# Kernel tuning notes

Hardware: AMD Instinct MI355X
Metric: run time of the kernel (lower is better)

Reference implementation:

```python
import jax, jax.numpy as jnp
import numpy as np

N_USERS = 100000
N_ENT = 100000
DIM = 64
HID = 128
E = 1600000
B = 8192


def _renorm(emb, max_norm=1.0):
    # torch nn.Embedding(max_norm=1): rows are rescaled to norm <= max_norm on lookup
    n = jnp.linalg.norm(emb, axis=-1, keepdims=True)
    return emb * jnp.minimum(1.0, max_norm / jnp.maximum(n, 1e-12))


def _gcn_conv(x, W, b, src, dst, n):
    # PyG GCNConv: h = x W; add self-loops; sym-normalized scatter-add; + bias
    h = x @ W  # [n, out]
    deg = jax.ops.segment_sum(jnp.ones(src.shape, jnp.float32), dst, num_segments=n) + 1.0  # self-loop
    dinv = jax.lax.rsqrt(deg)
    norm = (dinv[src] * dinv[dst])[:, None]  # [E,1]
    out = jax.ops.segment_sum(h[src] * norm, dst, num_segments=n)
    out = out + h * (1.0 / deg)[:, None]  # self-loop term: deg^-1/2 * deg^-1/2 = 1/deg
    return out + b


def setup_inputs() -> dict:
    key = jax.random.key(0)
    ks = jax.random.split(key, 8)
    return {
        "u": jax.random.randint(ks[0], (B,), 0, N_USERS),
        "i": jax.random.randint(ks[1], (B,), 0, N_ENT),
        "edges": jax.random.randint(ks[2], (2, E), 0, N_ENT),
        "user_emb": jax.random.normal(ks[3], (N_USERS, DIM), jnp.float32) * 0.1,
        "entity_emb": jax.random.normal(ks[4], (N_ENT, DIM), jnp.float32) * 0.1,
        "W1": jax.random.normal(ks[5], (DIM, HID), jnp.float32) * (1.0 / np.sqrt(DIM)),
        "b1": jnp.zeros((HID,), jnp.float32),
        "W2": jax.random.normal(ks[6], (HID, DIM), jnp.float32) * (1.0 / np.sqrt(HID)),
        "b2": jnp.zeros((DIM,), jnp.float32),
    }


def reference(u, i, edges, user_emb, entity_emb, W1, b1, W2, b2):
    src, dst = edges[0], edges[1]
    n = entity_emb.shape[0]
    x = _renorm(entity_emb)  # entitys(all_entitys_indexes) with max_norm=1
    x = jax.nn.relu(_gcn_conv(x, W1, b1, src, dst, n))  # dropout = identity (eval)
    x = _gcn_conv(x, W2, b2, src, dst, n)
    items = x[i]  # [B, DIM]
    users = _renorm(user_emb)[u]  # [B, DIM]
    uv = jnp.sum(users * items, axis=1)
    return jax.nn.sigmoid(uv)
```

## Files before the change

kernel.cpp:

```cpp
#include <hip/hip_runtime.h>
#include <hip/hip_bf16.h>
#include <math.h>

constexpr int N_ENT = 100000;
constexpr int NEDGE = 1600000;
constexpr int BATCH = 8192;

constexpr int NBUCK   = 256;
constexpr int KNODE   = 391;
constexpr int TILE    = 4096;
constexpr int NTILE   = (NEDGE + TILE - 1) / TILE;
constexpr int BUCKCAP = 8192;

constexpr int NBLK_G = (N_ENT + 63) / 64;
constexpr int ZROWS  = NBLK_G * 64;


typedef __attribute__((ext_vector_type(8))) short bf16x8;
typedef __attribute__((ext_vector_type(4))) float f32x4;

__device__ inline unsigned short f2b(float x) {
    unsigned int u = __float_as_uint(x);
    unsigned int r = (u + 0x7fffu + ((u >> 16) & 1u)) >> 16;
    return (unsigned short)r;
}
__device__ inline float blo(unsigned int p) { return __uint_as_float(p << 16); }
__device__ inline float bhi(unsigned int p) { return __uint_as_float(p & 0xffff0000u); }


__global__ __launch_bounds__(256) void prep_k(const float* __restrict__ emb,
                                              const int* __restrict__ degi,
                                              float* __restrict__ dinv,
                                              unsigned short* __restrict__ emb_b) {
    int gt   = blockIdx.x * 256 + threadIdx.x;
    int n    = gt >> 6;
    int lane = threadIdx.x & 63;
    if (n > N_ENT) return;
    if (n == N_ENT) { emb_b[(size_t)n * 64 + lane] = 0; return; }
    float v = emb[(size_t)n * 64 + lane];
    float s = v * v;
#pragma unroll
    for (int o = 32; o > 0; o >>= 1) s += __shfl_xor(s, o, 64);
    float nrm = sqrtf(s);
    float sc  = nrm > 1.0f ? 1.0f / nrm : 1.0f;
    float dv  = 1.0f / sqrtf((float)(degi[n] + 1));
    if (lane == 0) dinv[n] = dv;
    emb_b[(size_t)n * 64 + lane] = f2b(sc * dv * v);
}

__global__ __launch_bounds__(256) void init_k(const float* __restrict__ W1g,
                                              const float* __restrict__ W2g,
                                              uint4* __restrict__ w1p,
                                              uint4* __restrict__ w2p,
                                              int* __restrict__ gcursor) {
    if (blockIdx.x == 8) { gcursor[threadIdx.x] = threadIdx.x * BUCKCAP; return; }
    int t = blockIdx.x * 256 + threadIdx.x;
    int e    = t & 1023;
    int lane = e & 63, cs = e >> 6;
    int li   = lane & 15, quad = lane >> 4;
    unsigned short v[8];
    if (t < 1024) {
        int ct = cs >> 1, s = cs & 1;
        int kb = s * 32 + quad * 8;
        int n  = ct * 16 + li;
#pragma unroll
        for (int j = 0; j < 8; ++j) v[j] = f2b(W1g[(kb + j) * 128 + n]);
        uint4 p;
        p.x = (unsigned)v[0] | ((unsigned)v[1] << 16);
        p.y = (unsigned)v[2] | ((unsigned)v[3] << 16);
        p.z = (unsigned)v[4] | ((unsigned)v[5] << 16);
        p.w = (unsigned)v[6] | ((unsigned)v[7] << 16);
        w1p[e] = p;
    } else {
        int ct = cs >> 2, s = cs & 3;
        int kb = s * 32 + quad * 8;
        int n  = ct * 16 + li;
#pragma unroll
        for (int j = 0; j < 8; ++j) v[j] = f2b(W2g[(kb + j) * 64 + n]);
        uint4 p;
        p.x = (unsigned)v[0] | ((unsigned)v[1] << 16);
        p.y = (unsigned)v[2] | ((unsigned)v[3] << 16);
        p.z = (unsigned)v[4] | ((unsigned)v[5] << 16);
        p.w = (unsigned)v[6] | ((unsigned)v[7] << 16);
        w2p[e] = p;
    }
}

__global__ __launch_bounds__(256) void bin_k(const int* __restrict__ edges,
                                             int* __restrict__ gcursor,
                                             unsigned int* __restrict__ temp) {
    __shared__ int cnt[NBUCK];
    __shared__ int gb[NBUCK];
    __shared__ int off[NBUCK];
    int tid  = threadIdx.x;
    int base = blockIdx.x * TILE;
    unsigned int val[16];
    unsigned int bpk[4] = {0u, 0u, 0u, 0u};
    cnt[tid] = 0;
    __syncthreads();
#pragma unroll
    for (int i = 0; i < 16; ++i) {
        int e = base + i * 256 + tid;
        unsigned int b = 0u;
        if (e < NEDGE) {
            int s  = edges[e];
            int d  = edges[NEDGE + e];
            int bb = d / KNODE;
            int dl = d - bb * KNODE;
            val[i] = ((unsigned int)s << 9) | (unsigned int)dl;
            b = (unsigned int)bb;
            atomicAdd(&cnt[bb], 1);
        } else {
            val[i] = 0xffffffffu;
        }
        bpk[i >> 2] |= b << ((i & 3) * 8);
    }
    __syncthreads();
    if (cnt[tid] > 0) gb[tid] = atomicAdd(&gcursor[tid], cnt[tid]);
    off[tid] = 0;
    __syncthreads();
#pragma unroll
    for (int i = 0; i < 16; ++i) {
        if (val[i] != 0xffffffffu) {
            int b = (int)((bpk[i >> 2] >> ((i & 3) * 8)) & 255u);
            int p = atomicAdd(&off[b], 1);
            temp[gb[b] + p] = val[i];
        }
    }
}

__global__ __launch_bounds__(256) void count_k(const unsigned int* __restrict__ temp,
                                               const int* __restrict__ gcursor,
                                               int* __restrict__ degi) {
    __shared__ int cnt[KNODE];
    int b     = blockIdx.x;
    int node0 = b * KNODE;
    int nn    = N_ENT - node0; if (nn > KNODE) nn = KNODE;
    for (int i = threadIdx.x; i < KNODE; i += 256) cnt[i] = 0;
    __syncthreads();
    int tbeg = b * BUCKCAP;
    int tend = gcursor[b];
    for (int idx = tbeg + threadIdx.x; idx < tend; idx += 256)
        atomicAdd(&cnt[temp[idx] & 511u], 1);
    __syncthreads();
    for (int i = threadIdx.x; i < nn; i += 256) degi[node0 + i] = cnt[i];
}

__global__ __launch_bounds__(256) void scan_offsets(const int* __restrict__ gcursor,
                                                    int* __restrict__ bucket_base,
                                                    int* __restrict__ row_start) {
    __shared__ int ts[NBUCK];
    int t = threadIdx.x;
    int v = gcursor[t] - t * BUCKCAP;
    ts[t] = v;
    __syncthreads();
    for (int off = 1; off < NBUCK; off <<= 1) {
        int x = (t >= off) ? ts[t - off] : 0;
        __syncthreads();
        ts[t] += x;
        __syncthreads();
    }
    bucket_base[t] = ts[t] - v;
    if (t == 0) row_start[N_ENT] = NEDGE;
}

__global__ __launch_bounds__(256) void unbin_k(const unsigned int* __restrict__ temp,
                                               const int* __restrict__ gcursor,
                                               const int* __restrict__ bucket_base,
                                               const int* __restrict__ degi,
                                               int* __restrict__ row_start,
                                               int* __restrict__ srcs) {
    __shared__ int cur[KNODE];
    int b     = blockIdx.x;
    int node0 = b * KNODE;
    int nn    = N_ENT - node0; if (nn > KNODE) nn = KNODE;
    int tid   = threadIdx.x;
    if (tid < 64) {
        int lane = tid;
        int loc[7];
        int s = 0;
#pragma unroll
        for (int j = 0; j < 7; ++j) {
            int idx = lane * 7 + j;
            int d = (idx < nn) ? degi[node0 + idx] : 0;
            loc[j] = s;
            s += d;
        }
        int v = s;
#pragma unroll
        for (int o = 1; o < 64; o <<= 1) {
            int x = __shfl_up(v, o, 64);
            if (lane >= o) v += x;
        }
        int pfx  = v - s;
        int base = bucket_base[b];
#pragma unroll
        for (int j = 0; j < 7; ++j) {
            int idx = lane * 7 + j;
            if (idx < nn) {
                int rs = base + pfx + loc[j];
                cur[idx] = rs;
                row_start[node0 + idx] = rs;
            }
        }
    }
    __syncthreads();
    int tbeg = b * BUCKCAP;
    int tend = gcursor[b];
    for (int idx = tbeg + tid; idx < tend; idx += 256) {
        unsigned int v = temp[idx];
        int dl = (int)(v & 511u);
        int s  = (int)(v >> 9);
        int pos = atomicAdd(&cur[dl], 1);
        srcs[pos] = s;
    }
}

__global__ __launch_bounds__(256) void reduce1_k(const int* __restrict__ row_start,
                                                 const int* __restrict__ srcs,
                                                 const unsigned short* __restrict__ emb_b,
                                                 const float* __restrict__ dinv,
                                                 unsigned short* __restrict__ zb) {
    int gt   = blockIdx.x * 256 + threadIdx.x;
    int dst  = gt >> 6;
    int lane = threadIdx.x & 63;
    int sub  = lane >> 4;
    int li   = lane & 15;
    int beg = row_start[dst];
    int end = row_start[dst + 1];
    float4 acc = make_float4(0.f, 0.f, 0.f, 0.f);
    for (int base = beg; base < end; base += 64) {
        int cnt = end - base; if (cnt > 64) cnt = 64;
        int s_v = (base + lane < end) ? srcs[base + lane] : N_ENT;
        for (int jj = 0; jj < cnt; jj += 16) {
            int s0 = __shfl(s_v, jj + sub,      64);
            int s1 = __shfl(s_v, jj + 4 + sub,  64);
            int s2 = __shfl(s_v, jj + 8 + sub,  64);
            int s3 = __shfl(s_v, jj + 12 + sub, 64);
            uint2 p0 = *(const uint2*)(emb_b + (size_t)s0 * 64 + li * 4);
            uint2 p1 = *(const uint2*)(emb_b + (size_t)s1 * 64 + li * 4);
            uint2 p2 = *(const uint2*)(emb_b + (size_t)s2 * 64 + li * 4);
            uint2 p3 = *(const uint2*)(emb_b + (size_t)s3 * 64 + li * 4);
            acc.x += blo(p0.x) + blo(p1.x) + blo(p2.x) + blo(p3.x);
            acc.y += bhi(p0.x) + bhi(p1.x) + bhi(p2.x) + bhi(p3.x);
            acc.z += blo(p0.y) + blo(p1.y) + blo(p2.y) + blo(p3.y);
            acc.w += bhi(p0.y) + bhi(p1.y) + bhi(p2.y) + bhi(p3.y);
        }
    }
    acc.x += __shfl_xor(acc.x, 16, 64); acc.y += __shfl_xor(acc.y, 16, 64);
    acc.z += __shfl_xor(acc.z, 16, 64); acc.w += __shfl_xor(acc.w, 16, 64);
    acc.x += __shfl_xor(acc.x, 32, 64); acc.y += __shfl_xor(acc.y, 32, 64);
    acc.z += __shfl_xor(acc.z, 32, 64); acc.w += __shfl_xor(acc.w, 32, 64);
    if (lane < 16) {
        uint2 po = *(const uint2*)(emb_b + (size_t)dst * 64 + li * 4);
        float dv = dinv[dst];
        unsigned int h0 = f2b(dv * (acc.x + blo(po.x)));
        unsigned int h1 = f2b(dv * (acc.y + bhi(po.x)));
        unsigned int h2 = f2b(dv * (acc.z + blo(po.y)));
        unsigned int h3 = f2b(dv * (acc.w + bhi(po.y)));
        uint2 p;
        p.x = h0 | (h1 << 16);
        p.y = h2 | (h3 << 16);
        *(uint2*)(zb + (size_t)dst * 64 + li * 4) = p;
    }
}

__global__ __launch_bounds__(256) void mlp_k(const unsigned short* __restrict__ zb,
                                             const uint4* __restrict__ w1p,
                                             const float* __restrict__ b1,
                                             const uint4* __restrict__ w2p,
                                             const float* __restrict__ dinv,
                                             unsigned short* __restrict__ h2b) {
    __shared__ unsigned short y1s[4][16 * 136];
    __shared__ unsigned short h2s[4][16 * 64];
    int tid  = threadIdx.x;
    int w    = tid >> 6, lane = tid & 63;
    int li   = lane & 15, quad = lane >> 4;
    int r0   = blockIdx.x * 64 + w * 16;
    uint4 a0u = *(const uint4*)(zb + (size_t)(r0 + li) * 64 + quad * 8);
    uint4 a1u = *(const uint4*)(zb + (size_t)(r0 + li) * 64 + 32 + quad * 8);
    bf16x8 a0 = *(bf16x8*)&a0u;
    bf16x8 a1 = *(bf16x8*)&a1u;
    unsigned short* ys = y1s[w];
#pragma unroll
    for (int ct = 0; ct < 8; ++ct) {
        uint4 b0u = w1p[(ct * 2 + 0) * 64 + lane];
        uint4 b1u = w1p[(ct * 2 + 1) * 64 + lane];
        f32x4 acc = {0.f, 0.f, 0.f, 0.f};
        acc = __builtin_amdgcn_mfma_f32_16x16x32_bf16(a0, *(bf16x8*)&b0u, acc, 0, 0, 0);
        acc = __builtin_amdgcn_mfma_f32_16x16x32_bf16(a1, *(bf16x8*)&b1u, acc, 0, 0, 0);
        float bias = b1[ct * 16 + li];
#pragma unroll
        for (int r = 0; r < 4; ++r)
            ys[(quad * 4 + r) * 136 + ct * 16 + li] = f2b(fmaxf(acc[r] + bias, 0.f));
    }
    __syncthreads();
    bf16x8 a2[4];
#pragma unroll
    for (int s = 0; s < 4; ++s) {
        uint4 au = *(const uint4*)(ys + li * 136 + s * 32 + quad * 8);
        a2[s] = *(bf16x8*)&au;
    }
    float dvr[4];
#pragma unroll
    for (int r = 0; r < 4; ++r) {
        int grow = r0 + quad * 4 + r;
        dvr[r] = (grow < N_ENT) ? dinv[grow] : 0.f;
    }
    unsigned short* hs = h2s[w];
#pragma unroll
    for (int ct = 0; ct < 4; ++ct) {
        f32x4 acc = {0.f, 0.f, 0.f, 0.f};
#pragma unroll
        for (int s = 0; s < 4; ++s) {
            uint4 bu = w2p[(ct * 4 + s) * 64 + lane];
            acc = __builtin_amdgcn_mfma_f32_16x16x32_bf16(a2[s], *(bf16x8*)&bu, acc, 0, 0, 0);
        }
#pragma unroll
        for (int r = 0; r < 4; ++r)
            hs[(quad * 4 + r) * 64 + ct * 16 + li] = f2b(acc[r] * dvr[r]);
    }
    __syncthreads();
#pragma unroll
    for (int q = 0; q < 2; ++q) {
        int t4   = lane * 2 + q;
        int rl   = t4 >> 3;
        int c0   = (t4 & 7) * 8;
        int grow = r0 + rl;
        if (grow < N_ENT) {
            *(uint4*)(h2b + (size_t)grow * 64 + c0) = *(const uint4*)(hs + rl * 64 + c0);
        } else if (grow == N_ENT) {
            uint4 zz; zz.x = 0u; zz.y = 0u; zz.z = 0u; zz.w = 0u;
            *(uint4*)(h2b + (size_t)grow * 64 + c0) = zz;
        }
    }
}

__global__ __launch_bounds__(256) void reduce2f_k(const int* __restrict__ u,
                                                  const int* __restrict__ iidx,
                                                  const float* __restrict__ uemb,
                                                  const int* __restrict__ row_start,
                                                  const int* __restrict__ srcs,
                                                  const unsigned short* __restrict__ h2b,
                                                  const float* __restrict__ dinv,
                                                  const float* __restrict__ b2,
                                                  float* __restrict__ out) {
    int gt   = blockIdx.x * 256 + threadIdx.x;
    int b    = gt >> 6;
    int lane = threadIdx.x & 63;
    int sub  = lane >> 4;
    int li   = lane & 15;
    int dst = iidx[b];
    int beg = row_start[dst];
    int end = row_start[dst + 1];
    float4 acc = make_float4(0.f, 0.f, 0.f, 0.f);
    for (int base = beg; base < end; base += 64) {
        int cnt = end - base; if (cnt > 64) cnt = 64;
        int s_v = (base + lane < end) ? srcs[base + lane] : N_ENT;
        for (int jj = 0; jj < cnt; jj += 16) {
            int s0 = __shfl(s_v, jj + sub,      64);
            int s1 = __shfl(s_v, jj + 4 + sub,  64);
            int s2 = __shfl(s_v, jj + 8 + sub,  64);
            int s3 = __shfl(s_v, jj + 12 + sub, 64);
            uint2 p0 = *(const uint2*)(h2b + (size_t)s0 * 64 + li * 4);
            uint2 p1 = *(const uint2*)(h2b + (size_t)s1 * 64 + li * 4);
            uint2 p2 = *(const uint2*)(h2b + (size_t)s2 * 64 + li * 4);
            uint2 p3 = *(const uint2*)(h2b + (size_t)s3 * 64 + li * 4);
            acc.x += blo(p0.x) + blo(p1.x) + blo(p2.x) + blo(p3.x);
            acc.y += bhi(p0.x) + bhi(p1.x) + bhi(p2.x) + bhi(p3.x);
            acc.z += blo(p0.y) + blo(p1.y) + blo(p2.y) + blo(p3.y);
            acc.w += bhi(p0.y) + bhi(p1.y) + bhi(p2.y) + bhi(p3.y);
        }
    }
    acc.x += __shfl_xor(acc.x, 16, 64); acc.y += __shfl_xor(acc.y, 16, 64);
    acc.z += __shfl_xor(acc.z, 16, 64); acc.w += __shfl_xor(acc.w, 16, 64);
    acc.x += __shfl_xor(acc.x, 32, 64); acc.y += __shfl_xor(acc.y, 32, 64);
    acc.z += __shfl_xor(acc.z, 32, 64); acc.w += __shfl_xor(acc.w, 32, 64);
    float s1 = 0.f, s2 = 0.f;
    if (lane < 16) {
        uint2 po = *(const uint2*)(h2b + (size_t)dst * 64 + li * 4);
        float dv = dinv[dst];
        float4 bb = *(const float4*)(b2 + li * 4);
        float4 z2v;
        z2v.x = dv * (acc.x + blo(po.x)) + bb.x;
        z2v.y = dv * (acc.y + bhi(po.x)) + bb.y;
        z2v.z = dv * (acc.z + blo(po.y)) + bb.z;
        z2v.w = dv * (acc.w + bhi(po.y)) + bb.w;
        float4 ue = *(const float4*)(uemb + (size_t)u[b] * 64 + li * 4);
        s1 = ue.x * ue.x + ue.y * ue.y + ue.z * ue.z + ue.w * ue.w;
        s2 = ue.x * z2v.x + ue.y * z2v.y + ue.z * z2v.z + ue.w * z2v.w;
    }
#pragma unroll
    for (int o = 8; o > 0; o >>= 1) {
        s1 += __shfl_xor(s1, o, 64);
        s2 += __shfl_xor(s2, o, 64);
    }
    if (lane == 0) {
        float nrm = sqrtf(s1);
        float sc  = nrm > 1.0f ? 1.0f / nrm : 1.0f;
        float uv  = s2 * sc;
        out[b] = 1.0f / (1.0f + expf(-uv));
    }
}

extern "C" void kernel_launch(void* const* d_in, const int* in_sizes, int n_in,
                              void* d_out, int out_size, void* d_ws, size_t ws_size,
                              hipStream_t stream) {
    const int*   u          = (const int*)d_in[0];
    const int*   iidx       = (const int*)d_in[1];
    const int*   edges      = (const int*)d_in[2];
    const float* user_emb   = (const float*)d_in[3];
    const float* entity_emb = (const float*)d_in[4];
    const float* W1         = (const float*)d_in[5];
    const float* b1         = (const float*)d_in[6];
    const float* W2         = (const float*)d_in[7];
    const float* b2         = (const float*)d_in[8];
    float*       out        = (float*)d_out;

    char* ws = (char*)d_ws;
    int*            degi        = (int*)           (ws);
    float*          dinv        = (float*)         (ws + 100000u * 4);
    int*            row_start   = (int*)           (ws + 200000u * 4);
    int*            gcursor     = (int*)           (ws + 300004u * 4);
    int*            bucket_base = (int*)           (ws + 300264u * 4);
    uint4*          w1p         = (uint4*)         (ws + 300656u * 4);
    uint4*          w2p         = (uint4*)         (ws + 304752u * 4);
    int*            srcs        = (int*)           (ws + 308848u * 4);
    unsigned short* emb_b       = (unsigned short*)(ws + 1908848u * 4);
    unsigned short* zb          = (unsigned short*)(ws + 3508864u * 4);
    unsigned short* h2b         = (unsigned short*)(ws + 6711936u * 4);
    unsigned int*   temp        = (unsigned int*)  (ws + 8311968u * 4);

    init_k<<<9, 256, 0, stream>>>(W1, W2, w1p, w2p, gcursor);
    bin_k<<<NTILE, 256, 0, stream>>>(edges, gcursor, temp);
    count_k<<<NBUCK, 256, 0, stream>>>(temp, gcursor, degi);
    scan_offsets<<<1, 256, 0, stream>>>(gcursor, bucket_base, row_start);

    prep_k<<<N_ENT * 64 / 256 + 1, 256, 0, stream>>>(entity_emb, degi, dinv, emb_b);

    unbin_k<<<NBUCK, 256, 0, stream>>>(temp, gcursor, bucket_base, degi,
                                       row_start, srcs);

    reduce1_k<<<N_ENT * 64 / 256, 256, 0, stream>>>(row_start, srcs, emb_b, dinv, zb);
    mlp_k<<<NBLK_G, 256, 0, stream>>>(zb, w1p, b1, w2p, dinv, h2b);

    reduce2f_k<<<BATCH * 64 / 256, 256, 0, stream>>>(u, iidx, user_emb, row_start,
                                                     srcs, h2b, dinv, b2, out);
}
```

Before: 238.2 us.

## Fuse count, scan and unbin into one LDS-staged kernel; derive degree from row_start

Merges the per-bucket degree count, global bucket scan and unbin scatter into a single kernel. Each block recomputes the 256-entry prefix scan redundantly and stages its bucket in LDS, so temp is read once instead of twice. Weight packing moves into extra blocks of the same launch, and degrees are taken from row_start differences, which drops the degi array. This removes several launches and a global round trip, at the cost of 32KB LDS per block, which may lower occupancy. reduce1 is also split into two launches over halves of the nodes.

```diff
diff --git a/kernel.cpp b/kernel.cpp
--- a/kernel.cpp
+++ b/kernel.cpp
@@ -28,62 +28,8 @@
 __device__ inline float bhi(unsigned int p) { return __uint_as_float(p & 0xffff0000u); }
 
 
-__global__ __launch_bounds__(256) void prep_k(const float* __restrict__ emb,
-                                              const int* __restrict__ degi,
-                                              float* __restrict__ dinv,
-                                              unsigned short* __restrict__ emb_b) {
-    int gt   = blockIdx.x * 256 + threadIdx.x;
-    int n    = gt >> 6;
-    int lane = threadIdx.x & 63;
-    if (n > N_ENT) return;
-    if (n == N_ENT) { emb_b[(size_t)n * 64 + lane] = 0; return; }
-    float v = emb[(size_t)n * 64 + lane];
-    float s = v * v;
-#pragma unroll
-    for (int o = 32; o > 0; o >>= 1) s += __shfl_xor(s, o, 64);
-    float nrm = sqrtf(s);
-    float sc  = nrm > 1.0f ? 1.0f / nrm : 1.0f;
-    float dv  = 1.0f / sqrtf((float)(degi[n] + 1));
-    if (lane == 0) dinv[n] = dv;
-    emb_b[(size_t)n * 64 + lane] = f2b(sc * dv * v);
-}
-
-__global__ __launch_bounds__(256) void init_k(const float* __restrict__ W1g,
-                                              const float* __restrict__ W2g,
-                                              uint4* __restrict__ w1p,
-                                              uint4* __restrict__ w2p,
-                                              int* __restrict__ gcursor) {
-    if (blockIdx.x == 8) { gcursor[threadIdx.x] = threadIdx.x * BUCKCAP; return; }
-    int t = blockIdx.x * 256 + threadIdx.x;
-    int e    = t & 1023;
-    int lane = e & 63, cs = e >> 6;
-    int li   = lane & 15, quad = lane >> 4;
-    unsigned short v[8];
-    if (t < 1024) {
-        int ct = cs >> 1, s = cs & 1;
-        int kb = s * 32 + quad * 8;
-        int n  = ct * 16 + li;
-#pragma unroll
-        for (int j = 0; j < 8; ++j) v[j] = f2b(W1g[(kb + j) * 128 + n]);
-        uint4 p;
-        p.x = (unsigned)v[0] | ((unsigned)v[1] << 16);
-        p.y = (unsigned)v[2] | ((unsigned)v[3] << 16);
-        p.z = (unsigned)v[4] | ((unsigned)v[5] << 16);
-        p.w = (unsigned)v[6] | ((unsigned)v[7] << 16);
-        w1p[e] = p;
-    } else {
-        int ct = cs >> 2, s = cs & 3;
-        int kb = s * 32 + quad * 8;
-        int n  = ct * 16 + li;
-#pragma unroll
-        for (int j = 0; j < 8; ++j) v[j] = f2b(W2g[(kb + j) * 64 + n]);
-        uint4 p;
-        p.x = (unsigned)v[0] | ((unsigned)v[1] << 16);
-        p.y = (unsigned)v[2] | ((unsigned)v[3] << 16);
-        p.z = (unsigned)v[4] | ((unsigned)v[5] << 16);
-        p.w = (unsigned)v[6] | ((unsigned)v[7] << 16);
-        w2p[e] = p;
-    }
+__global__ __launch_bounds__(256) void ginit_k(int* __restrict__ gcursor) {
+    gcursor[threadIdx.x] = threadIdx.x * BUCKCAP;
 }
 
 __global__ __launch_bounds__(256) void bin_k(const int* __restrict__ edges,
@@ -129,52 +75,76 @@
     }
 }
 
-__global__ __launch_bounds__(256) void count_k(const unsigned int* __restrict__ temp,
-                                               const int* __restrict__ gcursor,
-                                               int* __restrict__ degi) {
+__global__ __launch_bounds__(256) void unbinC_k(const unsigned int* __restrict__ temp,
+                                                const int* __restrict__ gcursor,
+                                                const float* __restrict__ W1g,
+                                                const float* __restrict__ W2g,
+                                                uint4* __restrict__ w1p,
+                                                uint4* __restrict__ w2p,
+                                                int* __restrict__ row_start,
+                                                int* __restrict__ srcs) {
+    __shared__ unsigned int st[BUCKCAP];
+    __shared__ int bs[NBUCK];
     __shared__ int cnt[KNODE];
-    int b     = blockIdx.x;
+    __shared__ int cur[KNODE];
+    int b   = blockIdx.x;
+    int tid = threadIdx.x;
+    if (b >= NBUCK) {
+        int t    = (b - NBUCK) * 256 + tid;
+        int e    = t & 1023;
+        int lane = e & 63, cs = e >> 6;
+        int li   = lane & 15, quad = lane >> 4;
+        unsigned short v[8];
+        if (t < 1024) {
+            int ct = cs >> 1, s = cs & 1;
+            int kb = s * 32 + quad * 8;
+            int n  = ct * 16 + li;
+#pragma unroll
+            for (int j = 0; j < 8; ++j) v[j] = f2b(W1g[(kb + j) * 128 + n]);
+            uint4 p;
+            p.x = (unsigned)v[0] | ((unsigned)v[1] << 16);
+            p.y = (unsigned)v[2] | ((unsigned)v[3] << 16);
+            p.z = (unsigned)v[4] | ((unsigned)v[5] << 16);
+            p.w = (unsigned)v[6] | ((unsigned)v[7] << 16);
+            w1p[e] = p;
+        } else {
+            int ct = cs >> 2, s = cs & 3;
+            int kb = s * 32 + quad * 8;
+            int n  = ct * 16 + li;
+#pragma unroll
+            for (int j = 0; j < 8; ++j) v[j] = f2b(W2g[(kb + j) * 64 + n]);
+            uint4 p;
+            p.x = (unsigned)v[0] | ((unsigned)v[1] << 16);
+            p.y = (unsigned)v[2] | ((unsigned)v[3] << 16);
+            p.z = (unsigned)v[4] | ((unsigned)v[5] << 16);
+            p.w = (unsigned)v[6] | ((unsigned)v[7] << 16);
+            w2p[e] = p;
+        }
+        return;
+    }
+    int myc = gcursor[tid] - tid * BUCKCAP;
+    bs[tid] = myc;
+    __syncthreads();
+    for (int off = 1; off < NBUCK; off <<= 1) {
+        int x = (tid >= off) ? bs[tid - off] : 0;
+        __syncthreads();
+        bs[tid] += x;
+        __syncthreads();
+    }
     int node0 = b * KNODE;
     int nn    = N_ENT - node0; if (nn > KNODE) nn = KNODE;
-    for (int i = threadIdx.x; i < KNODE; i += 256) cnt[i] = 0;
-    __syncthreads();
-    int tbeg = b * BUCKCAP;
-    int tend = gcursor[b];
-    for (int idx = tbeg + threadIdx.x; idx < tend; idx += 256)
-        atomicAdd(&cnt[temp[idx] & 511u], 1);
-    __syncthreads();
-    for (int i = threadIdx.x; i < nn; i += 256) degi[node0 + i] = cnt[i];
-}
-
-__global__ __launch_bounds__(256) void scan_offsets(const int* __restrict__ gcursor,
-                                                    int* __restrict__ bucket_base,
-                                                    int* __restrict__ row_start) {
-    __shared__ int ts[NBUCK];
-    int t = threadIdx.x;
-    int v = gcursor[t] - t * BUCKCAP;
-    ts[t] = v;
-    __syncthreads();
-    for (int off = 1; off < NBUCK; off <<= 1) {
-        int x = (t >= off) ? ts[t - off] : 0;
-        __syncthreads();
-        ts[t] += x;
-        __syncthreads();
-    }
-    bucket_base[t] = ts[t] - v;
-    if (t == 0) row_start[N_ENT] = NEDGE;
-}
-
-__global__ __launch_bounds__(256) void unbin_k(const unsigned int* __restrict__ temp,
-                                               const int* __restrict__ gcursor,
-                                               const int* __restrict__ bucket_base,
-                                               const int* __restrict__ degi,
-                                               int* __restrict__ row_start,
-                                               int* __restrict__ srcs) {
-    __shared__ int cur[KNODE];
-    int b     = blockIdx.x;
-    int node0 = b * KNODE;
-    int nn    = N_ENT - node0; if (nn > KNODE) nn = KNODE;
-    int tid   = threadIdx.x;
+    int tbeg  = b * BUCKCAP;
+    int m     = gcursor[b] - tbeg;
+    int bucket_base = bs[b] - m;
+    for (int i = tid; i < KNODE; i += 256) cnt[i] = 0;
+    __syncthreads();
+    for (int i = tid; i < m; i += 256) {
+        unsigned int x = temp[tbeg + i];
+        st[i] = x;
+        atomicAdd(&cnt[x & 511u], 1);
+    }
+    if (b == 0 && tid == 255) row_start[N_ENT] = NEDGE;
+    __syncthreads();
     if (tid < 64) {
         int lane = tid;
         int loc[7];
@@ -182,7 +152,7 @@
 #pragma unroll
         for (int j = 0; j < 7; ++j) {
             int idx = lane * 7 + j;
-            int d = (idx < nn) ? degi[node0 + idx] : 0;
+            int d = (idx < nn) ? cnt[idx] : 0;
             loc[j] = s;
             s += d;
         }
@@ -192,37 +162,55 @@
             int x = __shfl_up(v, o, 64);
             if (lane >= o) v += x;
         }
-        int pfx  = v - s;
-        int base = bucket_base[b];
+        int pfx = v - s;
 #pragma unroll
         for (int j = 0; j < 7; ++j) {
             int idx = lane * 7 + j;
             if (idx < nn) {
-                int rs = base + pfx + loc[j];
+                int rs = bucket_base + pfx + loc[j];
                 cur[idx] = rs;
                 row_start[node0 + idx] = rs;
             }
         }
     }
     __syncthreads();
-    int tbeg = b * BUCKCAP;
-    int tend = gcursor[b];
-    for (int idx = tbeg + tid; idx < tend; idx += 256) {
-        unsigned int v = temp[idx];
-        int dl = (int)(v & 511u);
-        int s  = (int)(v >> 9);
+    for (int i = tid; i < m; i += 256) {
+        unsigned int x = st[i];
+        int dl  = (int)(x & 511u);
         int pos = atomicAdd(&cur[dl], 1);
-        srcs[pos] = s;
-    }
-}
-
-__global__ __launch_bounds__(256) void reduce1_k(const int* __restrict__ row_start,
+        srcs[pos] = (int)(x >> 9);
+    }
+}
+
+__global__ __launch_bounds__(256) void prep_k(const float* __restrict__ emb,
+                                              const int* __restrict__ row_start,
+                                              float* __restrict__ dinv,
+                                              unsigned short* __restrict__ emb_b) {
+    int gt   = blockIdx.x * 256 + threadIdx.x;
+    int n    = gt >> 6;
+    int lane = threadIdx.x & 63;
+    if (n > N_ENT) return;
+    if (n == N_ENT) { emb_b[(size_t)n * 64 + lane] = 0; return; }
+    float v = emb[(size_t)n * 64 + lane];
+    float s = v * v;
+#pragma unroll
+    for (int o = 32; o > 0; o >>= 1) s += __shfl_xor(s, o, 64);
+    float nrm = sqrtf(s);
+    float sc  = nrm > 1.0f ? 1.0f / nrm : 1.0f;
+    int   deg = row_start[n + 1] - row_start[n];
+    float dv  = 1.0f / sqrtf((float)(deg + 1));
+    if (lane == 0) dinv[n] = dv;
+    emb_b[(size_t)n * 64 + lane] = f2b(sc * dv * v);
+}
+
+__global__ __launch_bounds__(256) void reduce1_k(int dst0,
+                                                 const int* __restrict__ row_start,
                                                  const int* __restrict__ srcs,
                                                  const unsigned short* __restrict__ emb_b,
                                                  const float* __restrict__ dinv,
                                                  unsigned short* __restrict__ zb) {
     int gt   = blockIdx.x * 256 + threadIdx.x;
-    int dst  = gt >> 6;
+    int dst  = dst0 + (gt >> 6);
     int lane = threadIdx.x & 63;
     int sub  = lane >> 4;
     int li   = lane & 15;
@@ -418,30 +406,26 @@
     float*       out        = (float*)d_out;
 
     char* ws = (char*)d_ws;
-    int*            degi        = (int*)           (ws);
-    float*          dinv        = (float*)         (ws + 100000u * 4);
-    int*            row_start   = (int*)           (ws + 200000u * 4);
-    int*            gcursor     = (int*)           (ws + 300004u * 4);
-    int*            bucket_base = (int*)           (ws + 300264u * 4);
-    uint4*          w1p         = (uint4*)         (ws + 300656u * 4);
-    uint4*          w2p         = (uint4*)         (ws + 304752u * 4);
-    int*            srcs        = (int*)           (ws + 308848u * 4);
-    unsigned short* emb_b       = (unsigned short*)(ws + 1908848u * 4);
-    unsigned short* zb          = (unsigned short*)(ws + 3508864u * 4);
-    unsigned short* h2b         = (unsigned short*)(ws + 6711936u * 4);
-    unsigned int*   temp        = (unsigned int*)  (ws + 8311968u * 4);
-
-    init_k<<<9, 256, 0, stream>>>(W1, W2, w1p, w2p, gcursor);
+    float*          dinv      = (float*)         (ws + 100000u * 4);
+    int*            row_start = (int*)           (ws + 200000u * 4);
+    int*            gcursor   = (int*)           (ws + 300004u * 4);
+    uint4*          w1p       = (uint4*)         (ws + 300656u * 4);
+    uint4*          w2p       = (uint4*)         (ws + 304752u * 4);
+    int*            srcs      = (int*)           (ws + 308848u * 4);
+    unsigned short* emb_b     = (unsigned short*)(ws + 1908848u * 4);
+    unsigned short* zb        = (unsigned short*)(ws + 3508864u * 4);
+    unsigned short* h2b       = (unsigned short*)(ws + 6711936u * 4);
+    unsigned int*   temp      = (unsigned int*)  (ws + 8311968u * 4);
+
+    ginit_k<<<1, 256, 0, stream>>>(gcursor);
     bin_k<<<NTILE, 256, 0, stream>>>(edges, gcursor, temp);
-    count_k<<<NBUCK, 256, 0, stream>>>(temp, gcursor, degi);
-    scan_offsets<<<1, 256, 0, stream>>>(gcursor, bucket_base, row_start);
-
-    prep_k<<<N_ENT * 64 / 256 + 1, 256, 0, stream>>>(entity_emb, degi, dinv, emb_b);
-
-    unbin_k<<<NBUCK, 256, 0, stream>>>(temp, gcursor, bucket_base, degi,
-                                       row_start, srcs);
-
-    reduce1_k<<<N_ENT * 64 / 256, 256, 0, stream>>>(row_start, srcs, emb_b, dinv, zb);
+    unbinC_k<<<NBUCK + 8, 256, 0, stream>>>(temp, gcursor, W1, W2, w1p, w2p,
+                                            row_start, srcs);
+    prep_k<<<N_ENT * 64 / 256 + 1, 256, 0, stream>>>(entity_emb, row_start,
+                                                     dinv, emb_b);
+
+    reduce1_k<<<12500, 256, 0, stream>>>(0,     row_start, srcs, emb_b, dinv, zb);
+    reduce1_k<<<12500, 256, 0, stream>>>(50000, row_start, srcs, emb_b, dinv, zb);
     mlp_k<<<NBLK_G, 256, 0, stream>>>(zb, w1p, b1, w2p, dinv, h2b);
 
     reduce2f_k<<<BATCH * 64 / 256, 256, 0, stream>>>(u, iidx, user_emb, row_start,
```

Result: no change. 234.2 us (-1.7%).
